# Optimization experiments

Measured on AMD Instinct MI355X. Metric: run time of the kernel, lower is better.

The kernel has to match this reference:

```python
import jax, jax.numpy as jnp
import numpy as np

FRAME_LEN = 400
HOP = 160
FFT_LEN = 512
PREEMPH = 0.97
MEL_FLOOR = 1.192092955078125e-07


def _hertz_to_mel(freq):
    return 1127.0 * np.log(1.0 + freq / 700.0)


def _mel_filter_bank(num_frequency_bins=256, num_mel_filters=80, min_frequency=20.0,
                     max_frequency=8000.0, sampling_rate=16000):
    mel_min = _hertz_to_mel(min_frequency)
    mel_max = _hertz_to_mel(max_frequency)
    mel_freqs = np.linspace(mel_min, mel_max, num_mel_filters + 2)
    # NOTE: source has filter_freqs = mel_freqs (mel-space, intentional replication of bug)
    filter_freqs = mel_freqs
    fft_bin_width = sampling_rate / (num_frequency_bins * 2)
    fft_freqs = _hertz_to_mel(fft_bin_width * np.arange(num_frequency_bins))
    filter_diff = np.diff(filter_freqs)
    slopes = filter_freqs[None, :] - fft_freqs[:, None]          # [256, 82]
    down_slopes = -slopes[:, :-2] / filter_diff[:-1]
    up_slopes = slopes[:, 2:] / filter_diff[1:]
    fb = np.maximum(0.0, np.minimum(down_slopes, up_slopes))      # [256, 80]
    # F.pad(mel_filters, (0,0,0,1)) -> one extra zero row -> [257, 80]
    return np.pad(fb, ((0, 1), (0, 0))).astype(np.float32)


def _window():
    n = np.arange(FRAME_LEN)
    hann = 0.5 - 0.5 * np.cos(2.0 * np.pi * n / (FRAME_LEN - 1))  # periodic=False
    return (hann ** 0.85).astype(np.float32)


def setup_inputs() -> dict:
    key = jax.random.key(0)
    T = 9_600_000  # 10 min @ 16 kHz
    raw_speech = jax.random.normal(key, (1, T), dtype=jnp.float32)
    return {
        "raw_speech": raw_speech,
        "mel_filters": jnp.asarray(_mel_filter_bank()),  # [257, 80]
        "window": jnp.asarray(_window()),                # [400]
    }


def reference(raw_speech, mel_filters, window):
    wav = raw_speech.reshape(-1) * 32768.0  # * 2**15
    num_frames = 1 + (wav.shape[0] - FRAME_LEN) // HOP
    idx = jnp.arange(num_frames)[:, None] * HOP + jnp.arange(FRAME_LEN)[None, :]
    frames = wav[idx]                                         # [F, 400]
    frames = frames - frames.mean(axis=1, keepdims=True)      # remove DC offset
    # preemphasis: y[0] = x[0]*(1-p), y[n] = x[n] - p*x[n-1]
    pre = jnp.concatenate(
        [frames[:, :1] * (1.0 - PREEMPH), frames[:, 1:] - PREEMPH * frames[:, :-1]],
        axis=1,
    )
    pre = pre * window
    padded = jnp.pad(pre, ((0, 0), (0, FFT_LEN - FRAME_LEN)))  # [F, 512]
    spec = jnp.abs(jnp.fft.rfft(padded, axis=1)) ** 2          # [F, 257]
    mel = jnp.log(jnp.maximum(spec @ mel_filters, MEL_FLOOR))  # [F, 80]
    mean = mel.mean(axis=0, keepdims=True)
    var = mel.var(axis=0, keepdims=True, ddof=1)               # unbiased
    return (mel - mean) / jnp.sqrt(var + 1e-7)
```

## Files before the change

kernel.cpp:

```cpp
#include <hip/hip_runtime.h>
#include <math.h>

#define FRAME_LEN 400
#define HOP 160
#define NMEL 80
#define PREEMPH 0.97f
#define MEL_FLOOR 1.192092955078125e-07f
#define PPW 4
#define NSHADOW 8

__device__ __forceinline__ float2 cadd(float2 a, float2 b){ return make_float2(a.x+b.x, a.y+b.y); }
__device__ __forceinline__ float2 csub(float2 a, float2 b){ return make_float2(a.x-b.x, a.y-b.y); }
__device__ __forceinline__ float2 cmul(float2 a, float2 b){ return make_float2(a.x*b.x-a.y*b.y, a.x*b.y+a.y*b.x); }

__device__ __forceinline__ float bperm(int addr, float v) {
    return __int_as_float(__builtin_amdgcn_ds_bpermute(addr, __float_as_int(v)));
}
template<int C>
__device__ __forceinline__ float dppf(float v) {
    return __int_as_float(__builtin_amdgcn_update_dpp(0, __float_as_int(v), C, 0xF, 0xF, false));
}
__device__ __forceinline__ float wscan_add(float v) {
    v += __int_as_float(__builtin_amdgcn_update_dpp(0, __float_as_int(v), 0x111, 0xF, 0xF, false));
    v += __int_as_float(__builtin_amdgcn_update_dpp(0, __float_as_int(v), 0x112, 0xF, 0xF, false));
    v += __int_as_float(__builtin_amdgcn_update_dpp(0, __float_as_int(v), 0x114, 0xF, 0xF, false));
    v += __int_as_float(__builtin_amdgcn_update_dpp(0, __float_as_int(v), 0x118, 0xF, 0xF, false));
    v += __int_as_float(__builtin_amdgcn_update_dpp(0, __float_as_int(v), 0x142, 0xA, 0xF, false));
    v += __int_as_float(__builtin_amdgcn_update_dpp(0, __float_as_int(v), 0x143, 0xC, 0xF, false));
    return v;
}

__global__ __launch_bounds__(256) void setup_kernel(float* __restrict__ frtab,
                                                    int* __restrict__ kstab)
{
    __shared__ float uu[256];
    int t = threadIdx.x;
    const double mel_min = 1127.0 * log(1.0 + 20.0 / 700.0);
    const double mel_max = 1127.0 * log(1.0 + 8000.0 / 700.0);
    const double dstep = (mel_max - mel_min) / 81.0;
    {
        double fhz = 31.25 * (double)t;
        double m = 1127.0 * log(1.0 + fhz / 700.0);
        uu[t] = (float)((m - mel_min) / dstep);
    }
    __syncthreads();
    {
        float u = uu[t];
        frtab[t] = u - floorf(u);
    }
    if (t < 82) {
        double fhz = 700.0 * (exp((mel_min + (double)t * dstep) / 1127.0) - 1.0);
        int k = (int)ceil(fhz / 31.25);
        k = max(0, min(256, k));
        while (k > 0 && uu[k - 1] >= (float)t) --k;
        while (k < 256 && uu[k] < (float)t) ++k;
        kstab[t] = k;
    }
}

__global__ __launch_bounds__(64) void feat_kernel(
    const float* __restrict__ raw, const float* __restrict__ window,
    float* __restrict__ mel_out, double* __restrict__ accum,
    const float* __restrict__ frtab, const int* __restrict__ kstab, int F)
{
    __shared__ __align__(16) float wlds[FRAME_LEN];
    __shared__ __align__(16) float xu[560];
    __shared__ __align__(16) float pfx[2][256];

    const int l = threadIdx.x;

    for (int i = l; i < FRAME_LEN; i += 64) wlds[i] = window[i] * 32768.f;

    const int bl   = __brev((unsigned)l) >> 26;
    const int adrX = (l ^ 63) << 2;
    const int adr0 = ((64 - l) & 63) << 2;

    float2 dt[5];
    float  sg[6];
    #pragma unroll
    for (int j = 0; j < 6; ++j) {
        int d = 1 << j;
        sg[j] = (l & d) ? -1.f : 1.f;
        if (j >= 1) {
            float2 tw = make_float2(1.f, 0.f);
            if (l & d) {
                float tt = (float)(l & (d - 1));
                float ang = -3.1415926535897932f * tt / (float)d;
                sincosf(ang, &tw.y, &tw.x);
            }
            dt[j - 1] = tw;
        }
    }
    float2 w2[4];
    #pragma unroll
    for (int q = 1; q < 4; ++q) {
        float ang = -6.283185307179586f * (float)(bl * q) * (1.0f / 256.0f);
        sincosf(ang, &w2[q].y, &w2[q].x);
    }
    float2 wk[4];
    #pragma unroll
    for (int q = 0; q < 4; ++q) {
        int k = 4 * l + q;
        float ang = -3.1415926535897932f * (float)k * (1.0f / 256.0f);
        sincosf(ang, &wk[q].y, &wk[q].x);
    }

    float fr1[4];
    {
        float4 fv = *(const float4*)(frtab + 4 * l);
        fr1[0] = fv.x; fr1[1] = fv.y; fr1[2] = fv.z; fr1[3] = fv.w;
    }
    int a0 = kstab[l], b0 = kstab[l + 1], e0 = kstab[l + 2];
    int a1 = 1, b1 = 1, e1 = 1;
    if (l < 16) { a1 = kstab[64 + l]; b1 = kstab[65 + l]; e1 = kstab[66 + l]; }

    const int NP = (F + 1) >> 1;
    const int basePair = blockIdx.x * PPW;

    float acc_s0 = 0.f, acc_q0 = 0.f;
    float acc_s1 = 0.f, acc_q1 = 0.f;

    for (int fi = 0; fi < PPW; ++fi) {
        int P = basePair + fi;
        if (P >= NP) break;
        int fA = 2 * P;
        bool hasB = (fA + 1) < F;

        const float4* g4 = (const float4*)(raw + (size_t)fA * HOP);
        float4 a = g4[l];
        float4 b = make_float4(0.f, 0.f, 0.f, 0.f);
        float4 c = make_float4(0.f, 0.f, 0.f, 0.f);
        if (hasB || l < 36) b = g4[64 + l];
        if (hasB && l < 12) c = g4[128 + l];
        float as = a.x + a.y + a.z + a.w;
        float bs = b.x + b.y + b.z + b.w;
        float cs = c.x + c.y + c.z + c.w;
        float sA8 = as + (l < 36 ? bs : 0.f);
        float sB8 = (l >= 40 ? as : 0.f) + bs + cs;
        float totA = __int_as_float(__builtin_amdgcn_readlane(__float_as_int(wscan_add(sA8)), 63));
        float totB = __int_as_float(__builtin_amdgcn_readlane(__float_as_int(wscan_add(sB8)), 63));
        float KA = totA * (1.0f / (float)FRAME_LEN) * (1.0f - PREEMPH);
        float KB = totB * (1.0f / (float)FRAME_LEN) * (1.0f - PREEMPH);

        ((float4*)xu)[l] = a;
        ((float4*)xu)[64 + l] = b;
        if (l < 12) ((float4*)xu)[128 + l] = c;

        float2 Z[2][4];
        #pragma unroll
        for (int r = 0; r < 4; ++r) {
            int off = 128 * r + 2 * bl;
            if (off < FRAME_LEN) {
                float2 xA = *(const float2*)(xu + off);
                float2 xB = *(const float2*)(xu + 160 + off);
                float xm1A = (off == 0) ? xA.x : xu[off - 1];
                float xm1B = (off == 0) ? xB.x : xu[159 + off];
                float2 wn  = *(const float2*)(wlds + off);
                Z[0][r] = make_float2((fmaf(-PREEMPH, xm1A, xA.x) - KA) * wn.x,
                                      (fmaf(-PREEMPH, xA.x,  xA.y) - KA) * wn.y);
                Z[1][r] = make_float2((fmaf(-PREEMPH, xm1B, xB.x) - KB) * wn.x,
                                      (fmaf(-PREEMPH, xB.x,  xB.y) - KB) * wn.y);
            } else {
                Z[0][r] = make_float2(0.f, 0.f);
                Z[1][r] = make_float2(0.f, 0.f);
            }
        }

        #pragma unroll
        for (int s = 0; s < 2; ++s) {
            float2 t0 = cadd(Z[s][0], Z[s][2]);
            float2 t1 = csub(Z[s][0], Z[s][2]);
            float2 t2 = cadd(Z[s][1], Z[s][3]);
            float2 t3 = csub(Z[s][1], Z[s][3]);
            Z[s][0] = cadd(t0, t2);
            Z[s][2] = csub(t0, t2);
            Z[s][1] = make_float2(t1.x + t3.y, t1.y - t3.x);
            Z[s][3] = make_float2(t1.x - t3.y, t1.y + t3.x);
            #pragma unroll
            for (int q = 1; q < 4; ++q) Z[s][q] = cmul(Z[s][q], w2[q]);
        }

        #pragma unroll
        for (int s = 0; s < 2; ++s)
        #pragma unroll
        for (int q = 0; q < 4; ++q) {
            float ox = dppf<0xB1>(Z[s][q].x), oy = dppf<0xB1>(Z[s][q].y);
            Z[s][q].x = fmaf(sg[0], Z[s][q].x, ox);
            Z[s][q].y = fmaf(sg[0], Z[s][q].y, oy);
        }
        #pragma unroll
        for (int s = 0; s < 2; ++s)
        #pragma unroll
        for (int q = 0; q < 4; ++q) {
            float2 Zw = cmul(Z[s][q], dt[0]);
            float ox = dppf<0x4E>(Zw.x), oy = dppf<0x4E>(Zw.y);
            Z[s][q].x = fmaf(sg[1], Zw.x, ox);
            Z[s][q].y = fmaf(sg[1], Zw.y, oy);
        }
        #pragma unroll
        for (int s = 0; s < 2; ++s)
        #pragma unroll
        for (int q = 0; q < 4; ++q) {
            float2 Zw = cmul(Z[s][q], dt[1]);
            float ox = __shfl_xor(Zw.x, 4, 64), oy = __shfl_xor(Zw.y, 4, 64);
            Z[s][q].x = fmaf(sg[2], Zw.x, ox);
            Z[s][q].y = fmaf(sg[2], Zw.y, oy);
        }
        #pragma unroll
        for (int s = 0; s < 2; ++s)
        #pragma unroll
        for (int q = 0; q < 4; ++q) {
            float2 Zw = cmul(Z[s][q], dt[2]);
            float ox = dppf<0x128>(Zw.x), oy = dppf<0x128>(Zw.y);
            Z[s][q].x = fmaf(sg[3], Zw.x, ox);
            Z[s][q].y = fmaf(sg[3], Zw.y, oy);
        }
        #pragma unroll
        for (int s = 0; s < 2; ++s)
        #pragma unroll
        for (int q = 0; q < 4; ++q) {
            float2 Zw = cmul(Z[s][q], dt[3]);
            float ox = __shfl_xor(Zw.x, 16, 64), oy = __shfl_xor(Zw.y, 16, 64);
            Z[s][q].x = fmaf(sg[4], Zw.x, ox);
            Z[s][q].y = fmaf(sg[4], Zw.y, oy);
        }
        #pragma unroll
        for (int s = 0; s < 2; ++s)
        #pragma unroll
        for (int q = 0; q < 4; ++q) {
            float2 Zw = cmul(Z[s][q], dt[4]);
            float ox = __shfl_xor(Zw.x, 32, 64), oy = __shfl_xor(Zw.y, 32, 64);
            Z[s][q].x = fmaf(sg[5], Zw.x, ox);
            Z[s][q].y = fmaf(sg[5], Zw.y, oy);
        }

        #pragma unroll
        for (int s = 0; s < 2; ++s) {
            float zcr[4], zci[4];
            zcr[0] = bperm(adr0, Z[s][0].x);
            zci[0] = bperm(adr0, Z[s][0].y);
            zcr[1] = bperm(adrX, Z[s][3].x);
            zci[1] = bperm(adrX, Z[s][3].y);
            zcr[2] = bperm(adrX, Z[s][2].x);
            zci[2] = bperm(adrX, Z[s][2].y);
            zcr[3] = bperm(adrX, Z[s][1].x);
            zci[3] = bperm(adrX, Z[s][1].y);

            float pw[4], pv[4];
            #pragma unroll
            for (int q = 0; q < 4; ++q) {
                float Er = 0.5f * (Z[s][q].x + zcr[q]);
                float Ei = 0.5f * (Z[s][q].y - zci[q]);
                float Or = 0.5f * (Z[s][q].y + zci[q]);
                float Oi = 0.5f * (zcr[q] - Z[s][q].x);
                float Xr = Er + Or * wk[q].x - Oi * wk[q].y;
                float Xi = Ei + Or * wk[q].y + Oi * wk[q].x;
                pw[q] = Xr * Xr + Xi * Xi;
                pv[q] = pw[q] * fr1[q];
            }
            float A0 = pw[0], A1 = A0 + pw[1], A2 = A1 + pw[2], A3 = A2 + pw[3];
            float B0 = pv[0], B1 = B0 + pv[1], B2 = B1 + pv[2], B3 = B2 + pv[3];
            float sA = wscan_add(A3);
            float sB = wscan_add(B3);
            float exA = sA - A3;
            float exB = sB - B3;
            float* pP = pfx[0];
            float* pF = pfx[1];
            ((float4*)pP)[l] = make_float4(exA + A0, exA + A1, exA + A2, exA + A3);
            ((float4*)pF)[l] = make_float4(exB + B0, exB + B1, exB + B2, exB + B3);

            int f = fA + s;
            bool act = (s == 0) || hasB;
            if (act) {
                float E1a = pF[a0 - 1], E1b = pF[b0 - 1], E1e = pF[e0 - 1];
                float EAb = pP[b0 - 1], EAe = pP[e0 - 1];
                float acc = fmaf(2.f, E1b, -E1a) - E1e + (EAe - EAb);
                float v = __logf(fmaxf(acc, MEL_FLOOR));
                mel_out[(size_t)f * NMEL + l] = v;
                acc_s0 += v; acc_q0 = fmaf(v, v, acc_q0);
                if (l < 16) {
                    float F1a = pF[a1 - 1], F1b = pF[b1 - 1], F1e = pF[e1 - 1];
                    float FAb = pP[b1 - 1], FAe = pP[e1 - 1];
                    float ac2 = fmaf(2.f, F1b, -F1a) - F1e + (FAe - FAb);
                    float v1 = __logf(fmaxf(ac2, MEL_FLOOR));
                    mel_out[(size_t)f * NMEL + 64 + l] = v1;
                    acc_s1 += v1; acc_q1 = fmaf(v1, v1, acc_q1);
                }
            }
        }
    }

    double* A = accum + (blockIdx.x & (NSHADOW - 1)) * 160;
    atomicAdd(&A[l], (double)acc_s0);
    atomicAdd(&A[80 + l], (double)acc_q0);
    if (l < 16) {
        atomicAdd(&A[64 + l], (double)acc_s1);
        atomicAdd(&A[144 + l], (double)acc_q1);
    }
}

__global__ __launch_bounds__(256) void norm_kernel(
    float* __restrict__ mel, const double* __restrict__ accum, int F)
{
    __shared__ float s_mean[NMEL], s_inv[NMEL];
    int t = threadIdx.x;
    if (t < NMEL) {
        double S = 0.0, Q = 0.0;
        #pragma unroll
        for (int j = 0; j < NSHADOW; ++j) {
            S += accum[j * 160 + t];
            Q += accum[j * 160 + 80 + t];
        }
        double mean = S / (double)F;
        double var = (Q - S * S / (double)F) / (double)(F - 1);
        s_mean[t] = (float)mean;
        s_inv[t]  = (float)(1.0 / sqrt(var + 1e-7));
    }
    __syncthreads();
    unsigned n = (unsigned)F * NMEL;
    unsigned stride = gridDim.x * 256u * 4u;
    unsigned i = (blockIdx.x * 256u + (unsigned)t) * 4u;
    int c = (int)(i % NMEL);
    float m0 = s_mean[c],     r0 = s_inv[c];
    float m1 = s_mean[c + 1], r1 = s_inv[c + 1];
    float m2 = s_mean[c + 2], r2 = s_inv[c + 2];
    float m3 = s_mean[c + 3], r3 = s_inv[c + 3];
    for (; i < n; i += stride) {
        float4 v = *(float4*)(mel + i);
        v.x = (v.x - m0) * r0;
        v.y = (v.y - m1) * r1;
        v.z = (v.z - m2) * r2;
        v.w = (v.w - m3) * r3;
        *(float4*)(mel + i) = v;
    }
}

extern "C" void kernel_launch(void* const* d_in, const int* in_sizes, int n_in,
                              void* d_out, int out_size, void* d_ws, size_t ws_size,
                              hipStream_t stream)
{
    const float* raw = (const float*)d_in[0];
    const float* window = (const float*)d_in[2];
    float* out = (float*)d_out;

    int N = in_sizes[0];
    int F = 1 + (N - FRAME_LEN) / HOP;

    double* accum = (double*)d_ws;
    float*  frtab = (float*)((char*)d_ws + NSHADOW * 160 * sizeof(double));
    int*    kstab = (int*)((char*)d_ws + NSHADOW * 160 * sizeof(double) + 256 * sizeof(float));

    hipMemsetAsync(d_ws, 0, NSHADOW * 160 * sizeof(double), stream);
    setup_kernel<<<1, 256, 0, stream>>>(frtab, kstab);
    int NP = (F + 1) / 2;
    int gridA = (NP + PPW - 1) / PPW;
    feat_kernel<<<gridA, 64, 0, stream>>>(raw, window, out, accum, frtab, kstab, F);
    norm_kernel<<<2560, 256, 0, stream>>>(out, accum, F);
}
```

Baseline: 150.0 us.

## Fold DC removal into spectrum via window DFT table and use permlane swaps

Precomputes the DFT of the scaled window in a widened setup kernel, so the per-frame mean is subtracted in the frequency domain with one FMA per bin instead of before the FFT. This lets the mean reduction overlap with the FFT rather than block the windowing step. When available, the last two FFT butterfly stages use permlane16/32 swap instructions instead of xor shuffles. It adds setup work and a table load per frame, and may change rounding slightly.

```diff
diff --git a/kernel.cpp b/kernel.cpp
--- a/kernel.cpp
+++ b/kernel.cpp
@@ -8,6 +8,15 @@
 #define MEL_FLOOR 1.192092955078125e-07f
 #define PPW 4
 #define NSHADOW 8
+
+#ifndef __has_builtin
+#define __has_builtin(x) 0
+#endif
+#if __has_builtin(__builtin_amdgcn_permlane16_swap) && __has_builtin(__builtin_amdgcn_permlane32_swap)
+#define USE_PLSWAP 1
+#else
+#define USE_PLSWAP 0
+#endif
 
 __device__ __forceinline__ float2 cadd(float2 a, float2 b){ return make_float2(a.x+b.x, a.y+b.y); }
 __device__ __forceinline__ float2 csub(float2 a, float2 b){ return make_float2(a.x-b.x, a.y-b.y); }
@@ -30,38 +39,96 @@
     return v;
 }
 
-__global__ __launch_bounds__(256) void setup_kernel(float* __restrict__ frtab,
-                                                    int* __restrict__ kstab)
+#if USE_PLSWAP
+typedef unsigned int uint2v __attribute__((ext_vector_type(2)));
+__device__ __forceinline__ void bflytw16(float2& A, float2& B, float2 tw) {
+    uint2v sx = __builtin_amdgcn_permlane16_swap(__float_as_uint(A.x), __float_as_uint(B.x), false, false);
+    uint2v sy = __builtin_amdgcn_permlane16_swap(__float_as_uint(A.y), __float_as_uint(B.y), false, false);
+    float lx = __uint_as_float(sx.x), hx = __uint_as_float(sx.y);
+    float ly = __uint_as_float(sy.x), hy = __uint_as_float(sy.y);
+    float cr = tw.x * hx - tw.y * hy;
+    float ci = tw.x * hy + tw.y * hx;
+    float r1x = lx + cr, r2x = lx - cr;
+    float r1y = ly + ci, r2y = ly - ci;
+    uint2v tx = __builtin_amdgcn_permlane16_swap(__float_as_uint(r1x), __float_as_uint(r2x), false, false);
+    uint2v ty = __builtin_amdgcn_permlane16_swap(__float_as_uint(r1y), __float_as_uint(r2y), false, false);
+    A = make_float2(__uint_as_float(tx.x), __uint_as_float(ty.x));
+    B = make_float2(__uint_as_float(tx.y), __uint_as_float(ty.y));
+}
+__device__ __forceinline__ void bflytw32(float2& A, float2& B, float2 tw) {
+    uint2v sx = __builtin_amdgcn_permlane32_swap(__float_as_uint(A.x), __float_as_uint(B.x), false, false);
+    uint2v sy = __builtin_amdgcn_permlane32_swap(__float_as_uint(A.y), __float_as_uint(B.y), false, false);
+    float lx = __uint_as_float(sx.x), hx = __uint_as_float(sx.y);
+    float ly = __uint_as_float(sy.x), hy = __uint_as_float(sy.y);
+    float cr = tw.x * hx - tw.y * hy;
+    float ci = tw.x * hy + tw.y * hx;
+    float r1x = lx + cr, r2x = lx - cr;
+    float r1y = ly + ci, r2y = ly - ci;
+    uint2v tx = __builtin_amdgcn_permlane32_swap(__float_as_uint(r1x), __float_as_uint(r2x), false, false);
+    uint2v ty = __builtin_amdgcn_permlane32_swap(__float_as_uint(r1y), __float_as_uint(r2y), false, false);
+    A = make_float2(__uint_as_float(tx.x), __uint_as_float(ty.x));
+    B = make_float2(__uint_as_float(tx.y), __uint_as_float(ty.y));
+}
+#endif
+
+__global__ __launch_bounds__(256) void setup_kernel(const float* __restrict__ window,
+                                                    float* __restrict__ frtab,
+                                                    int* __restrict__ kstab,
+                                                    float* __restrict__ wftab)
 {
-    __shared__ float uu[256];
-    int t = threadIdx.x;
-    const double mel_min = 1127.0 * log(1.0 + 20.0 / 700.0);
-    const double mel_max = 1127.0 * log(1.0 + 8000.0 / 700.0);
-    const double dstep = (mel_max - mel_min) / 81.0;
-    {
-        double fhz = 31.25 * (double)t;
-        double m = 1127.0 * log(1.0 + fhz / 700.0);
-        uu[t] = (float)((m - mel_min) / dstep);
-    }
-    __syncthreads();
-    {
-        float u = uu[t];
-        frtab[t] = u - floorf(u);
-    }
-    if (t < 82) {
-        double fhz = 700.0 * (exp((mel_min + (double)t * dstep) / 1127.0) - 1.0);
-        int k = (int)ceil(fhz / 31.25);
-        k = max(0, min(256, k));
-        while (k > 0 && uu[k - 1] >= (float)t) --k;
-        while (k < 256 && uu[k] < (float)t) ++k;
-        kstab[t] = k;
+    const int bid = blockIdx.x;
+    const int t = threadIdx.x;
+    if (bid == 0) {
+        __shared__ float uu[256];
+        const double mel_min = 1127.0 * log(1.0 + 20.0 / 700.0);
+        const double mel_max = 1127.0 * log(1.0 + 8000.0 / 700.0);
+        const double dstep = (mel_max - mel_min) / 81.0;
+        {
+            double fhz = 31.25 * (double)t;
+            double m = 1127.0 * log(1.0 + fhz / 700.0);
+            uu[t] = (float)((m - mel_min) / dstep);
+        }
+        __syncthreads();
+        {
+            float u = uu[t];
+            frtab[t] = u - floorf(u);
+        }
+        if (t < 82) {
+            double fhz = 700.0 * (exp((mel_min + (double)t * dstep) / 1127.0) - 1.0);
+            int k = (int)ceil(fhz / 31.25);
+            k = max(0, min(256, k));
+            while (k > 0 && uu[k - 1] >= (float)t) --k;
+            while (k < 256 && uu[k] < (float)t) ++k;
+            kstab[t] = k;
+        }
+    } else {
+        if (t >= 64) return;
+        const int k = bid - 1;
+        float sr = 0.f, si = 0.f;
+        #pragma unroll
+        for (int j = 0; j < 7; ++j) {
+            int n = t + 64 * j;
+            if (n < FRAME_LEN) {
+                float wv = window[n] * 32768.f;
+                int m = (k * n) & 511;
+                float ang = -3.1415926535897932f * (float)m * (1.0f / 256.0f);
+                float sv, cv;
+                sincosf(ang, &sv, &cv);
+                sr = fmaf(wv, cv, sr);
+                si = fmaf(wv, sv, si);
+            }
+        }
+        sr = wscan_add(sr);
+        si = wscan_add(si);
+        if (t == 63) { wftab[2 * k] = sr; wftab[2 * k + 1] = si; }
     }
 }
 
 __global__ __launch_bounds__(64) void feat_kernel(
     const float* __restrict__ raw, const float* __restrict__ window,
     float* __restrict__ mel_out, double* __restrict__ accum,
-    const float* __restrict__ frtab, const int* __restrict__ kstab, int F)
+    const float* __restrict__ frtab, const int* __restrict__ kstab,
+    const float* __restrict__ wftab, int F)
 {
     __shared__ __align__(16) float wlds[FRAME_LEN];
     __shared__ __align__(16) float xu[560];
@@ -75,6 +142,31 @@
     const int adrX = (l ^ 63) << 2;
     const int adr0 = ((64 - l) & 63) << 2;
 
+#if USE_PLSWAP
+    float2 dt[3];
+    float  sg[4];
+    #pragma unroll
+    for (int j = 0; j < 4; ++j) {
+        int d = 1 << j;
+        sg[j] = (l & d) ? -1.f : 1.f;
+        if (j >= 1) {
+            float2 tw = make_float2(1.f, 0.f);
+            if (l & d) {
+                float tt = (float)(l & (d - 1));
+                float ang = -3.1415926535897932f * tt / (float)d;
+                sincosf(ang, &tw.y, &tw.x);
+            }
+            dt[j - 1] = tw;
+        }
+    }
+    float2 tw16, tw32;
+    {
+        float a16 = -3.1415926535897932f * (float)(l & 15) * (1.0f / 16.0f);
+        float a32 = -3.1415926535897932f * (float)(l & 31) * (1.0f / 32.0f);
+        sincosf(a16, &tw16.y, &tw16.x);
+        sincosf(a32, &tw32.y, &tw32.x);
+    }
+#else
     float2 dt[5];
     float  sg[6];
     #pragma unroll
@@ -91,6 +183,7 @@
             dt[j - 1] = tw;
         }
     }
+#endif
     float2 w2[4];
     #pragma unroll
     for (int q = 1; q < 4; ++q) {
@@ -132,6 +225,10 @@
         float4 c = make_float4(0.f, 0.f, 0.f, 0.f);
         if (hasB || l < 36) b = g4[64 + l];
         if (hasB && l < 12) c = g4[128 + l];
+        ((float4*)xu)[l] = a;
+        ((float4*)xu)[64 + l] = b;
+        if (l < 12) ((float4*)xu)[128 + l] = c;
+
         float as = a.x + a.y + a.z + a.w;
         float bs = b.x + b.y + b.z + b.w;
         float cs = c.x + c.y + c.z + c.w;
@@ -142,10 +239,6 @@
         float KA = totA * (1.0f / (float)FRAME_LEN) * (1.0f - PREEMPH);
         float KB = totB * (1.0f / (float)FRAME_LEN) * (1.0f - PREEMPH);
 
-        ((float4*)xu)[l] = a;
-        ((float4*)xu)[64 + l] = b;
-        if (l < 12) ((float4*)xu)[128 + l] = c;
-
         float2 Z[2][4];
         #pragma unroll
         for (int r = 0; r < 4; ++r) {
@@ -156,10 +249,10 @@
                 float xm1A = (off == 0) ? xA.x : xu[off - 1];
                 float xm1B = (off == 0) ? xB.x : xu[159 + off];
                 float2 wn  = *(const float2*)(wlds + off);
-                Z[0][r] = make_float2((fmaf(-PREEMPH, xm1A, xA.x) - KA) * wn.x,
-                                      (fmaf(-PREEMPH, xA.x,  xA.y) - KA) * wn.y);
-                Z[1][r] = make_float2((fmaf(-PREEMPH, xm1B, xB.x) - KB) * wn.x,
-                                      (fmaf(-PREEMPH, xB.x,  xB.y) - KB) * wn.y);
+                Z[0][r] = make_float2(fmaf(-PREEMPH, xm1A, xA.x) * wn.x,
+                                      fmaf(-PREEMPH, xA.x,  xA.y) * wn.y);
+                Z[1][r] = make_float2(fmaf(-PREEMPH, xm1B, xB.x) * wn.x,
+                                      fmaf(-PREEMPH, xB.x,  xB.y) * wn.y);
             } else {
                 Z[0][r] = make_float2(0.f, 0.f);
                 Z[1][r] = make_float2(0.f, 0.f);
@@ -215,6 +308,18 @@
             Z[s][q].x = fmaf(sg[3], Zw.x, ox);
             Z[s][q].y = fmaf(sg[3], Zw.y, oy);
         }
+#if USE_PLSWAP
+        #pragma unroll
+        for (int s = 0; s < 2; ++s) {
+            bflytw16(Z[s][0], Z[s][1], tw16);
+            bflytw16(Z[s][2], Z[s][3], tw16);
+        }
+        #pragma unroll
+        for (int s = 0; s < 2; ++s) {
+            bflytw32(Z[s][0], Z[s][1], tw32);
+            bflytw32(Z[s][2], Z[s][3], tw32);
+        }
+#else
         #pragma unroll
         for (int s = 0; s < 2; ++s)
         #pragma unroll
@@ -233,9 +338,16 @@
             Z[s][q].x = fmaf(sg[5], Zw.x, ox);
             Z[s][q].y = fmaf(sg[5], Zw.y, oy);
         }
+#endif
+
+        float4 wfa = ((const float4*)wftab)[2 * l];
+        float4 wfb = ((const float4*)wftab)[2 * l + 1];
+        float wfr[4] = { wfa.x, wfa.z, wfb.x, wfb.z };
+        float wfi[4] = { wfa.y, wfa.w, wfb.y, wfb.w };
 
         #pragma unroll
         for (int s = 0; s < 2; ++s) {
+            float Ks = (s == 0) ? KA : KB;
             float zcr[4], zci[4];
             zcr[0] = bperm(adr0, Z[s][0].x);
             zci[0] = bperm(adr0, Z[s][0].y);
@@ -255,6 +367,8 @@
                 float Oi = 0.5f * (zcr[q] - Z[s][q].x);
                 float Xr = Er + Or * wk[q].x - Oi * wk[q].y;
                 float Xi = Ei + Or * wk[q].y + Oi * wk[q].x;
+                Xr = fmaf(-Ks, wfr[q], Xr);
+                Xi = fmaf(-Ks, wfi[q], Xi);
                 pw[q] = Xr * Xr + Xi * Xi;
                 pv[q] = pw[q] * fr1[q];
             }
@@ -348,12 +462,13 @@
 
     double* accum = (double*)d_ws;
     float*  frtab = (float*)((char*)d_ws + NSHADOW * 160 * sizeof(double));
-    int*    kstab = (int*)((char*)d_ws + NSHADOW * 160 * sizeof(double) + 256 * sizeof(float));
+    int*    kstab = (int*)((char*)d_ws + 11264);
+    float*  wftab = (float*)((char*)d_ws + 11776);
 
     hipMemsetAsync(d_ws, 0, NSHADOW * 160 * sizeof(double), stream);
-    setup_kernel<<<1, 256, 0, stream>>>(frtab, kstab);
+    setup_kernel<<<257, 256, 0, stream>>>(window, frtab, kstab, wftab);
     int NP = (F + 1) / 2;
     int gridA = (NP + PPW - 1) / PPW;
-    feat_kernel<<<gridA, 64, 0, stream>>>(raw, window, out, accum, frtab, kstab, F);
+    feat_kernel<<<gridA, 64, 0, stream>>>(raw, window, out, accum, frtab, kstab, wftab, F);
     norm_kernel<<<2560, 256, 0, stream>>>(out, accum, F);
 }
```

Result: faster. 141.4 us (-5.7%).
